# Kernel tuning notes

Hardware: AMD Instinct MI355X
Metric: run time of the kernel (lower is better)

The kernel has to match this reference:

```python
import jax, jax.numpy as jnp
import numpy as np

N_HEAD = 8
DQK = 64
DV = 64
D_IN = 512
D_OUT = 512
D_MID = 2048
B = 4
L = 2048
EPS = 1e-5


def layernorm(x):
    mu = jnp.mean(x, axis=-1, keepdims=True)
    var = jnp.mean(jnp.square(x - mu), axis=-1, keepdims=True)
    return (x - mu) / jnp.sqrt(var + EPS)


def setup_inputs() -> dict:
    key = jax.random.key(0)
    ks = jax.random.split(key, 10)
    s = 0.02
    return {
        "query": jax.random.normal(ks[0], (B, L, D_IN), jnp.float32),
        "key": jax.random.normal(ks[1], (B, L, D_IN), jnp.float32),
        "value": jax.random.normal(ks[2], (B, L, D_IN), jnp.float32),
        "mask": jnp.zeros((B, L, L), jnp.float32),
        "WQ": jax.random.normal(ks[3], (D_IN, N_HEAD * DQK), jnp.float32) * s,
        "WK": jax.random.normal(ks[4], (D_IN, N_HEAD * DQK), jnp.float32) * s,
        "WV": jax.random.normal(ks[5], (D_IN, N_HEAD * DV), jnp.float32) * s,
        "WO": jax.random.normal(ks[6], (N_HEAD * DV, D_OUT), jnp.float32) * s,
        "W1": jax.random.normal(ks[7], (D_OUT, D_MID), jnp.float32) * s,
        "W2": jax.random.normal(ks[8], (D_MID, D_OUT), jnp.float32) * s,
    }


def reference(query, key, value, mask, WQ, WK, WV, WO, W1, W2):
    bsz = query.shape[0]
    # projections -> [b, h, l, d]
    Q = (query @ WQ).reshape(bsz, -1, N_HEAD, DQK).transpose(0, 2, 1, 3)
    K = (key @ WK).reshape(bsz, -1, N_HEAD, DQK).transpose(0, 2, 1, 3)
    V = (value @ WV).reshape(bsz, -1, N_HEAD, DV).transpose(0, 2, 1, 3)
    # scaled dot-product attention with additive mask [b, 1, lq, lk]
    scores = jnp.einsum("bhqd,bhkd->bhqk", Q, K) / jnp.sqrt(jnp.float32(DQK))
    w = jax.nn.softmax(scores + mask[:, None, :, :], axis=-1)
    out = jnp.einsum("bhqk,bhkd->bhqd", w, V)
    out = out.transpose(0, 2, 1, 3).reshape(bsz, -1, N_HEAD * DV)
    out = out @ WO
    out = layernorm(query + out)
    ff = jax.nn.relu(out @ W1) @ W2
    return layernorm(out + ff)
```

## Files before the change

kernel.cpp:

```cpp
#include <hip/hip_runtime.h>
#include <hip/hip_bf16.h>

using bf16 = __bf16;
typedef __bf16 bf16x4 __attribute__((ext_vector_type(4)));
typedef __bf16 bf16x8 __attribute__((ext_vector_type(8)));
typedef float f32x4 __attribute__((ext_vector_type(4)));

static constexpr int BATCH = 4;
static constexpr int SEQ   = 2048;
static constexpr int DIN   = 512;
static constexpr int NHEAD = 8;
static constexpr int DMID  = 2048;
static constexpr int MROWS = BATCH * SEQ;

__device__ __forceinline__ void gload16(const void* g, void* l)
{
    __builtin_amdgcn_global_load_lds(
        (const __attribute__((address_space(1))) unsigned int*)g,
        (__attribute__((address_space(3))) unsigned int*)l, 16, 0, 0);
}

__global__ __launch_bounds__(256) void mask_check(const uint4* __restrict__ m,
                                                  int* __restrict__ flag)
{
    const int base = (blockIdx.x * 256 + threadIdx.x) * 4;
    unsigned nz = 0;
    for (int i = 0; i < 4; ++i) {
        const uint4 v = m[base + i];
        nz |= v.x | v.y | v.z | v.w;
    }
    if (nz) atomicOr(flag, 1);
}

__global__ __launch_bounds__(256) void transpose_weights(
    const float* __restrict__ WQ, const float* __restrict__ WK,
    const float* __restrict__ WV, const float* __restrict__ WO,
    const float* __restrict__ W1, const float* __restrict__ W2,
    bf16* __restrict__ WQt, bf16* __restrict__ WKt, bf16* __restrict__ WVt,
    bf16* __restrict__ WOt, bf16* __restrict__ W1t, bf16* __restrict__ W2t)
{
    __shared__ float tile[32][33];
    const int bid = blockIdx.x;
    const float* in; bf16* out; int ip, op, cx, ry;
    if (bid < 1024) {
        const int w = bid >> 8, idx = bid & 255;
        in  = w == 0 ? WQ  : w == 1 ? WK  : w == 2 ? WV  : WO;
        out = w == 0 ? WQt : w == 1 ? WKt : w == 2 ? WVt : WOt;
        ip = 512; op = 512; cx = idx & 15; ry = idx >> 4;
    } else if (bid < 2048) {
        const int idx = bid - 1024;
        in = W1; out = W1t; ip = 2048; op = 512; cx = idx & 63; ry = idx >> 6;
    } else {
        const int idx = bid - 2048;
        in = W2; out = W2t; ip = 512; op = 2048; cx = idx & 15; ry = idx >> 4;
    }
    const int c0 = cx * 32, r0 = ry * 32;
    const int tx = threadIdx.x & 31, ty = threadIdx.x >> 5;
    for (int i = 0; i < 32; i += 8)
        tile[ty + i][tx] = in[(size_t)(r0 + ty + i) * ip + c0 + tx];
    __syncthreads();
    for (int i = 0; i < 32; i += 8)
        out[(size_t)(c0 + ty + i) * op + r0 + tx] = (bf16)tile[tx][ty + i];
}

__global__ __launch_bounds__(256) void transpose_b2b(const bf16* __restrict__ in,
                                                     bf16* __restrict__ out,
                                                     int ip, int op)
{
    __shared__ bf16 tile[32][33];
    const int c0 = blockIdx.x * 32;
    const int r0 = blockIdx.y * 32;
    const int tx = threadIdx.x & 31;
    const int ty = threadIdx.x >> 5;
    for (int i = 0; i < 32; i += 8)
        tile[ty + i][tx] = in[(size_t)(r0 + ty + i) * ip + c0 + tx];
    __syncthreads();
    for (int i = 0; i < 32; i += 8)
        out[(size_t)(c0 + ty + i) * op + r0 + tx] = tile[tx][ty + i];
}

template <int ACT, bool AF32>
__device__ __forceinline__ void gemm128_body(const void* __restrict__ Ain,
                                             const bf16* __restrict__ Bt,
                                             bf16* __restrict__ C,
                                             int N, int K,
                                             bf16* sA, bf16* sB)
{
    const int t    = threadIdx.x;
    const int lane = t & 63;
    const int wave = t >> 6;
    const int wm   = wave >> 1;
    const int wn   = wave & 1;
    const int lr   = lane & 15;
    const int lq   = lane >> 4;

    const int m0 = blockIdx.y * 128;
    const int n0 = blockIdx.x * 128;

    const int srow = lane >> 3;
    const int scol = (lane & 7) * 8;

    f32x4 acc[4][4] = {};

    for (int k0 = 0; k0 < K; k0 += 64) {
        if constexpr (AF32) {
            const float* Af = (const float*)Ain;
            float4 fa[8];
#pragma unroll
            for (int i = 0; i < 4; ++i) {
                const float* p = Af + (size_t)(m0 + (wave * 4 + i) * 8 + srow) * K + k0 + scol;
                fa[2 * i]     = *reinterpret_cast<const float4*>(p);
                fa[2 * i + 1] = *reinterpret_cast<const float4*>(p + 4);
            }
            if (k0) __syncthreads();
#pragma unroll
            for (int i = 0; i < 4; ++i) {
                const int ch = wave * 4 + i;
                gload16(Bt + (size_t)(n0 + ch * 8 + srow) * K + k0 + scol, sB + ch * 512);
            }
#pragma unroll
            for (int i = 0; i < 4; ++i) {
                const int r = (wave * 4 + i) * 8 + srow;
                const float4 a = fa[2 * i], b = fa[2 * i + 1];
                bf16x8 h;
                h[0] = (bf16)a.x; h[1] = (bf16)a.y; h[2] = (bf16)a.z; h[3] = (bf16)a.w;
                h[4] = (bf16)b.x; h[5] = (bf16)b.y; h[6] = (bf16)b.z; h[7] = (bf16)b.w;
                *reinterpret_cast<bf16x8*>(&sA[r * 64 + scol]) = h;
            }
        } else {
            const bf16* Ab = (const bf16*)Ain;
            if (k0) __syncthreads();
#pragma unroll
            for (int i = 0; i < 4; ++i) {
                const int ch = wave * 4 + i;
                const int r  = ch * 8 + srow;
                gload16(Ab + (size_t)(m0 + r) * K + k0 + scol, sA + ch * 512);
                gload16(Bt + (size_t)(n0 + r) * K + k0 + scol, sB + ch * 512);
            }
        }
        __syncthreads();

#pragma unroll
        for (int kk = 0; kk < 2; ++kk) {
            bf16x8 af[4], bfr[4];
#pragma unroll
            for (int x = 0; x < 4; ++x) {
                af[x]  = *reinterpret_cast<const bf16x8*>(&sA[(wm * 64 + x * 16 + lr) * 64 + kk * 32 + lq * 8]);
                bfr[x] = *reinterpret_cast<const bf16x8*>(&sB[(wn * 64 + x * 16 + lr) * 64 + kk * 32 + lq * 8]);
            }
#pragma unroll
            for (int m = 0; m < 4; ++m)
#pragma unroll
                for (int n = 0; n < 4; ++n)
                    acc[m][n] = __builtin_amdgcn_mfma_f32_16x16x32_bf16(af[m], bfr[n], acc[m][n], 0, 0, 0);
        }
    }

#pragma unroll
    for (int n = 0; n < 4; ++n) {
        const int col = n0 + wn * 64 + n * 16 + lr;
#pragma unroll
        for (int m = 0; m < 4; ++m) {
            const int rowb = m0 + wm * 64 + m * 16 + lq * 4;
#pragma unroll
            for (int j = 0; j < 4; ++j) {
                float v = acc[m][n][j];
                if (ACT == 1) v = v > 0.f ? v : 0.f;
                C[(size_t)(rowb + j) * N + col] = (bf16)v;
            }
        }
    }
}

template <int ACT>
__global__ __launch_bounds__(256) void gemm128(const bf16* __restrict__ A,
                                               const bf16* __restrict__ Bt,
                                               bf16* __restrict__ C,
                                               int N, int K)
{
    __shared__ bf16 sA[128 * 64];
    __shared__ bf16 sB[128 * 64];
    gemm128_body<ACT, false>(A, Bt, C, N, K, sA, sB);
}

__global__ __launch_bounds__(256) void gemm128_qkv(const float* __restrict__ q,
                                                   const float* __restrict__ k,
                                                   const float* __restrict__ v,
                                                   const bf16* __restrict__ WQt,
                                                   const bf16* __restrict__ WKt,
                                                   const bf16* __restrict__ WVt,
                                                   bf16* __restrict__ Qb,
                                                   bf16* __restrict__ Kb,
                                                   bf16* __restrict__ Vb)
{
    __shared__ bf16 sA[128 * 64];
    __shared__ bf16 sB[128 * 64];
    const void* A  = blockIdx.z == 0 ? (const void*)q : blockIdx.z == 1 ? (const void*)k : (const void*)v;
    const bf16* Bt = blockIdx.z == 0 ? WQt : blockIdx.z == 1 ? WKt : WVt;
    bf16*       C  = blockIdx.z == 0 ? Qb  : blockIdx.z == 1 ? Kb  : Vb;
    gemm128_body<0, true>(A, Bt, C, DIN, DIN, sA, sB);
}

__global__ __launch_bounds__(256) void attn_kernel(const bf16* __restrict__ Qb,
                                                   const bf16* __restrict__ Kb,
                                                   const bf16* __restrict__ Vt,
                                                   const float* __restrict__ mask,
                                                   bf16* __restrict__ O,
                                                   const int* __restrict__ mzf)
{
    const int bi   = blockIdx.x;
    const int xcd  = bi & 7;
    const int slot = bi >> 3;
    const int pair = xcd * 4 + (slot >> 5);
    const int qt   = slot & 31;
    const int h    = pair >> 2;
    const int b    = pair & 3;

    const int t    = threadIdx.x;
    const int lane = t & 63;
    const int wave = t >> 6;
    const int lr   = lane & 15;
    const int lq   = lane >> 4;
    const int q0   = qt * 64;
    const bool useM = (*mzf != 0);

    __shared__ bf16 sK[64 * 72];
    __shared__ bf16 sV[64 * 72];
    __shared__ bf16 sP[4][16 * 72];
    __shared__ bf16 sM[64 * 68];

    const int  qrow = q0 + wave * 16 + lr;
    const bf16* qp  = Qb + (size_t)(b * SEQ + qrow) * DIN + h * 64 + lq * 8;
    const bf16x8 qf0 = *reinterpret_cast<const bf16x8*>(qp);
    const bf16x8 qf1 = *reinterpret_cast<const bf16x8*>(qp + 32);

    f32x4 o[4] = {};
    f32x4 lrow = {};

    const int sr = t >> 2;
    const int sc = (t & 3) << 3;

    const bf16*  kbase = Kb + (size_t)(b * SEQ) * DIN + h * 64;
    const bf16*  vbase = Vt + (size_t)(h * 64 + sr) * MROWS + b * SEQ;
    const float* mbase = mask + ((size_t)b * SEQ + q0) * SEQ;

    constexpr float L2E = 1.4426950408889634f;
    constexpr float SCL = 0.125f * L2E;
    const bf16x8 ones = {(bf16)1.f, (bf16)1.f, (bf16)1.f, (bf16)1.f,
                         (bf16)1.f, (bf16)1.f, (bf16)1.f, (bf16)1.f};

    int4 kr0 = *reinterpret_cast<const int4*>(kbase + (size_t)sr * DIN + sc);
    int4 kr1 = *reinterpret_cast<const int4*>(kbase + (size_t)sr * DIN + sc + 32);
    int4 vr0 = *reinterpret_cast<const int4*>(vbase + sc);
    int4 vr1 = *reinterpret_cast<const int4*>(vbase + sc + 32);

    for (int tile = 0; tile < SEQ / 64; ++tile) {
        if (tile) __syncthreads();

        *reinterpret_cast<int4*>(&sK[sr * 72 + sc])      = kr0;
        *reinterpret_cast<int4*>(&sK[sr * 72 + sc + 32]) = kr1;
        *reinterpret_cast<int4*>(&sV[sr * 72 + sc])      = vr0;
        *reinterpret_cast<int4*>(&sV[sr * 72 + sc + 32]) = vr1;
        if (useM) {
            const int k0 = tile * 64;
            for (int i = 0; i < 4; ++i) {
                const int idx = t + 256 * i;
                const float4 mr = *reinterpret_cast<const float4*>(
                    mbase + (size_t)(idx >> 4) * SEQ + k0 + (idx & 15) * 4);
                bf16x4 mv;
                mv[0] = (bf16)(mr.x * L2E); mv[1] = (bf16)(mr.y * L2E);
                mv[2] = (bf16)(mr.z * L2E); mv[3] = (bf16)(mr.w * L2E);
                *reinterpret_cast<bf16x4*>(&sM[(idx >> 4) * 68 + (idx & 15) * 4]) = mv;
            }
        }

        if (tile + 1 < SEQ / 64) {
            const int k0 = (tile + 1) * 64;
            kr0 = *reinterpret_cast<const int4*>(kbase + (size_t)(k0 + sr) * DIN + sc);
            kr1 = *reinterpret_cast<const int4*>(kbase + (size_t)(k0 + sr) * DIN + sc + 32);
            vr0 = *reinterpret_cast<const int4*>(vbase + k0 + sc);
            vr1 = *reinterpret_cast<const int4*>(vbase + k0 + sc + 32);
        }
        __syncthreads();

        f32x4 sf[4] = {};
        for (int s = 0; s < 2; ++s) {
            const bf16x8 qf = s ? qf1 : qf0;
            for (int ni = 0; ni < 4; ++ni) {
                bf16x8 kf = *reinterpret_cast<const bf16x8*>(&sK[(ni * 16 + lr) * 72 + s * 32 + lq * 8]);
                sf[ni] = __builtin_amdgcn_mfma_f32_16x16x32_bf16(qf, kf, sf[ni], 0, 0, 0);
            }
        }

        if (useM) {
            for (int j = 0; j < 4; ++j) {
                const int mr2 = (wave * 16 + lq * 4 + j) * 68;
                for (int ni = 0; ni < 4; ++ni) {
                    const float mval = (float)sM[mr2 + ni * 16 + lr];
                    sP[wave][(lq * 4 + j) * 72 + ni * 16 + lr] = (bf16)exp2f(sf[ni][j] * SCL + mval);
                }
            }
        } else {
            for (int j = 0; j < 4; ++j)
                for (int ni = 0; ni < 4; ++ni)
                    sP[wave][(lq * 4 + j) * 72 + ni * 16 + lr] = (bf16)exp2f(sf[ni][j] * SCL);
        }

        f32x4 rs = {};
        for (int s = 0; s < 2; ++s) {
            bf16x8 pf = *reinterpret_cast<const bf16x8*>(&sP[wave][lr * 72 + s * 32 + lq * 8]);
            rs = __builtin_amdgcn_mfma_f32_16x16x32_bf16(pf, ones, rs, 0, 0, 0);
            for (int ni = 0; ni < 4; ++ni) {
                bf16x8 vf = *reinterpret_cast<const bf16x8*>(&sV[(ni * 16 + lr) * 72 + s * 32 + lq * 8]);
                o[ni] = __builtin_amdgcn_mfma_f32_16x16x32_bf16(pf, vf, o[ni], 0, 0, 0);
            }
        }
        for (int j = 0; j < 4; ++j)
            lrow[j] += rs[j];
    }

    for (int ni = 0; ni < 4; ++ni)
        for (int j = 0; j < 4; ++j) {
            const int row = q0 + wave * 16 + lq * 4 + j;
            const int col = h * 64 + ni * 16 + lr;
            O[(size_t)(b * SEQ + row) * DIN + col] = (bf16)(o[ni][j] / lrow[j]);
        }
}

__global__ __launch_bounds__(256) void add_ln(const float* __restrict__ X,
                                              const bf16* __restrict__ Y,
                                              bf16* __restrict__ Ob,
                                              float* __restrict__ Of)
{
    const int row  = blockIdx.x * 4 + (threadIdx.x >> 6);
    const int lane = threadIdx.x & 63;
    const size_t base = (size_t)row * DIN + lane * 8;
    const float4 x0 = *reinterpret_cast<const float4*>(X + base);
    const float4 x1 = *reinterpret_cast<const float4*>(X + base + 4);
    const bf16x8 yv = *reinterpret_cast<const bf16x8*>(Y + base);
    float v[8] = {x0.x, x0.y, x0.z, x0.w, x1.x, x1.y, x1.z, x1.w};
    float s = 0.f;
    for (int i = 0; i < 8; ++i) { v[i] += (float)yv[i]; s += v[i]; }
    for (int off = 1; off < 64; off <<= 1) s += __shfl_xor(s, off);
    const float mu = s * (1.f / DIN);
    float var = 0.f;
    for (int i = 0; i < 8; ++i) { const float d = v[i] - mu; var += d * d; }
    for (int off = 1; off < 64; off <<= 1) var += __shfl_xor(var, off);
    const float rstd = rsqrtf(var * (1.f / DIN) + 1e-5f);
    float r[8];
    for (int i = 0; i < 8; ++i) r[i] = (v[i] - mu) * rstd;
    if (Ob) {
        bf16x8 ov;
        for (int i = 0; i < 8; ++i) ov[i] = (bf16)r[i];
        *reinterpret_cast<bf16x8*>(Ob + base) = ov;
    }
    if (Of) {
        *reinterpret_cast<float4*>(Of + base)     = make_float4(r[0], r[1], r[2], r[3]);
        *reinterpret_cast<float4*>(Of + base + 4) = make_float4(r[4], r[5], r[6], r[7]);
    }
}

extern "C" void kernel_launch(void* const* d_in, const int* in_sizes, int n_in,
                              void* d_out, int out_size, void* d_ws, size_t ws_size,
                              hipStream_t stream)
{
    const float* query = (const float*)d_in[0];
    const float* key   = (const float*)d_in[1];
    const float* value = (const float*)d_in[2];
    const float* mask  = (const float*)d_in[3];
    const float* WQ    = (const float*)d_in[4];
    const float* WK    = (const float*)d_in[5];
    const float* WV    = (const float*)d_in[6];
    const float* WO    = (const float*)d_in[7];
    const float* W1    = (const float*)d_in[8];
    const float* W2    = (const float*)d_in[9];

    char* w = (char*)d_ws;
    size_t off = 0;
    auto carve2 = [&](size_t elems) { bf16* p = (bf16*)(w + off); off += elems * 2; return p; };
    auto carve4 = [&](size_t elems) { float* p = (float*)(w + off); off += elems * 4; return p; };

    bf16* Qb    = carve2((size_t)MROWS * DIN);
    bf16* Kb    = carve2((size_t)MROWS * DIN);
    bf16* Vb    = carve2((size_t)MROWS * DIN);
    bf16* Vt    = carve2((size_t)MROWS * DIN);
    bf16* Mid   = carve2((size_t)MROWS * DMID);
    float* Ln1f = carve4((size_t)MROWS * DIN);
    bf16* WQt   = carve2((size_t)DIN * DIN);
    bf16* WKt   = carve2((size_t)DIN * DIN);
    bf16* WVt   = carve2((size_t)DIN * DIN);
    bf16* WOt   = carve2((size_t)DIN * DIN);
    bf16* W1t   = carve2((size_t)DIN * DMID);
    bf16* W2t   = carve2((size_t)DMID * DIN);
    int*  mzf   = (int*)(w + off); off += 16;
    if (off > ws_size) return;

    bf16* Ob   = Vb;
    bf16* Two  = Qb;
    bf16* Ln1b = Kb;
    bf16* F2   = Vt;

    const dim3 blk(256);

    hipMemsetAsync(mzf, 0, 4, stream);
    mask_check<<<dim3(4096), blk, 0, stream>>>((const uint4*)mask, mzf);

    transpose_weights<<<dim3(3072), blk, 0, stream>>>(WQ, WK, WV, WO, W1, W2,
                                                      WQt, WKt, WVt, WOt, W1t, W2t);

    gemm128_qkv<<<dim3(DIN / 128, MROWS / 128, 3), blk, 0, stream>>>(query, key, value,
                                                                     WQt, WKt, WVt, Qb, Kb, Vb);

    transpose_b2b<<<dim3(DIN / 32, MROWS / 32), blk, 0, stream>>>(Vb, Vt, DIN, MROWS);

    attn_kernel<<<dim3(1024), blk, 0, stream>>>(Qb, Kb, Vt, mask, Ob, mzf);

    gemm128<0><<<dim3(DIN / 128, MROWS / 128), blk, 0, stream>>>(Ob, WOt, Two, DIN, DIN);
    add_ln<<<dim3(MROWS / 4), blk, 0, stream>>>(query, Two, Ln1b, Ln1f);

    gemm128<1><<<dim3(DMID / 128, MROWS / 128), blk, 0, stream>>>(Ln1b, W1t, Mid, DMID, DIN);
    gemm128<0><<<dim3(DIN / 128, MROWS / 128), blk, 0, stream>>>(Mid, W2t, F2, DIN, DMID);

    add_ln<<<dim3(MROWS / 4), blk, 0, stream>>>(Ln1f, F2, (bf16*)nullptr, (float*)d_out);
}
```

Before: 372.7 us.

## Use 64-row GEMM tiles for narrow GEMMs and 128-query attention tiles

Adds a 64x128 GEMM variant used for the QKV projection, the output projection and the W2 GEMM. For N=512 outputs this doubles the block count, which improves occupancy across the many CUs. The attention kernel now gives each wave 32 query rows instead of 16. Each loaded K/V tile and its register fragments are then reused twice, and the grid is halved to 512 blocks. The trade-offs are higher register and LDS pressure in attention, and fewer attention blocks than the CU count may leave some CUs idle.

After: 367.6 us. No clear change (-1.4%).

```diff
diff --git a/kernel.cpp b/kernel.cpp
--- a/kernel.cpp
+++ b/kernel.cpp
@@ -79,13 +79,15 @@
         out[(size_t)(c0 + ty + i) * op + r0 + tx] = tile[tx][ty + i];
 }
 
-template <int ACT, bool AF32>
-__device__ __forceinline__ void gemm128_body(const void* __restrict__ Ain,
-                                             const bf16* __restrict__ Bt,
-                                             bf16* __restrict__ C,
-                                             int N, int K,
-                                             bf16* sA, bf16* sB)
-{
+template <int ACT>
+__global__ __launch_bounds__(256) void gemm128(const bf16* __restrict__ A,
+                                               const bf16* __restrict__ Bt,
+                                               bf16* __restrict__ C,
+                                               int N, int K)
+{
+    __shared__ bf16 sA[128 * 64];
+    __shared__ bf16 sB[128 * 64];
+
     const int t    = threadIdx.x;
     const int lane = t & 63;
     const int wave = t >> 6;
@@ -103,40 +105,13 @@
     f32x4 acc[4][4] = {};
 
     for (int k0 = 0; k0 < K; k0 += 64) {
-        if constexpr (AF32) {
-            const float* Af = (const float*)Ain;
-            float4 fa[8];
-#pragma unroll
-            for (int i = 0; i < 4; ++i) {
-                const float* p = Af + (size_t)(m0 + (wave * 4 + i) * 8 + srow) * K + k0 + scol;
-                fa[2 * i]     = *reinterpret_cast<const float4*>(p);
-                fa[2 * i + 1] = *reinterpret_cast<const float4*>(p + 4);
-            }
-            if (k0) __syncthreads();
-#pragma unroll
-            for (int i = 0; i < 4; ++i) {
-                const int ch = wave * 4 + i;
-                gload16(Bt + (size_t)(n0 + ch * 8 + srow) * K + k0 + scol, sB + ch * 512);
-            }
-#pragma unroll
-            for (int i = 0; i < 4; ++i) {
-                const int r = (wave * 4 + i) * 8 + srow;
-                const float4 a = fa[2 * i], b = fa[2 * i + 1];
-                bf16x8 h;
-                h[0] = (bf16)a.x; h[1] = (bf16)a.y; h[2] = (bf16)a.z; h[3] = (bf16)a.w;
-                h[4] = (bf16)b.x; h[5] = (bf16)b.y; h[6] = (bf16)b.z; h[7] = (bf16)b.w;
-                *reinterpret_cast<bf16x8*>(&sA[r * 64 + scol]) = h;
-            }
-        } else {
-            const bf16* Ab = (const bf16*)Ain;
-            if (k0) __syncthreads();
-#pragma unroll
-            for (int i = 0; i < 4; ++i) {
-                const int ch = wave * 4 + i;
-                const int r  = ch * 8 + srow;
-                gload16(Ab + (size_t)(m0 + r) * K + k0 + scol, sA + ch * 512);
-                gload16(Bt + (size_t)(n0 + r) * K + k0 + scol, sB + ch * 512);
-            }
+        if (k0) __syncthreads();
+#pragma unroll
+        for (int i = 0; i < 4; ++i) {
+            const int ch = wave * 4 + i;
+            const int r  = ch * 8 + srow;
+            gload16(A  + (size_t)(m0 + r) * K + k0 + scol, sA + ch * 512);
+            gload16(Bt + (size_t)(n0 + r) * K + k0 + scol, sB + ch * 512);
         }
         __syncthreads();
 
@@ -172,33 +147,128 @@
     }
 }
 
+template <int ACT, bool AF32>
+__device__ __forceinline__ void gemm64_body(const void* __restrict__ Ain,
+                                            const bf16* __restrict__ Bt,
+                                            bf16* __restrict__ C,
+                                            int N, int K,
+                                            bf16* sA, bf16* sB)
+{
+    const int t    = threadIdx.x;
+    const int lane = t & 63;
+    const int wave = t >> 6;
+    const int lr   = lane & 15;
+    const int lq   = lane >> 4;
+
+    const int m0 = blockIdx.y * 64;
+    const int n0 = blockIdx.x * 128;
+
+    const int srow = lane >> 3;
+    const int scol = (lane & 7) * 8;
+
+    f32x4 acc[4][2] = {};
+
+    for (int k0 = 0; k0 < K; k0 += 64) {
+        if constexpr (AF32) {
+            const float* Af = (const float*)Ain;
+            float4 fa[4];
+#pragma unroll
+            for (int i = 0; i < 2; ++i) {
+                const float* p = Af + (size_t)(m0 + (wave * 2 + i) * 8 + srow) * K + k0 + scol;
+                fa[2 * i]     = *reinterpret_cast<const float4*>(p);
+                fa[2 * i + 1] = *reinterpret_cast<const float4*>(p + 4);
+            }
+            if (k0) __syncthreads();
+#pragma unroll
+            for (int i = 0; i < 4; ++i) {
+                const int ch = wave * 4 + i;
+                gload16(Bt + (size_t)(n0 + ch * 8 + srow) * K + k0 + scol, sB + ch * 512);
+            }
+#pragma unroll
+            for (int i = 0; i < 2; ++i) {
+                const int r = (wave * 2 + i) * 8 + srow;
+                const float4 a = fa[2 * i], b = fa[2 * i + 1];
+                bf16x8 hh;
+                hh[0] = (bf16)a.x; hh[1] = (bf16)a.y; hh[2] = (bf16)a.z; hh[3] = (bf16)a.w;
+                hh[4] = (bf16)b.x; hh[5] = (bf16)b.y; hh[6] = (bf16)b.z; hh[7] = (bf16)b.w;
+                *reinterpret_cast<bf16x8*>(&sA[r * 64 + scol]) = hh;
+            }
+        } else {
+            const bf16* Ab = (const bf16*)Ain;
+            if (k0) __syncthreads();
+#pragma unroll
+            for (int i = 0; i < 2; ++i) {
+                const int ch = wave * 2 + i;
+                gload16(Ab + (size_t)(m0 + ch * 8 + srow) * K + k0 + scol, sA + ch * 512);
+            }
+#pragma unroll
+            for (int i = 0; i < 4; ++i) {
+                const int ch = wave * 4 + i;
+                gload16(Bt + (size_t)(n0 + ch * 8 + srow) * K + k0 + scol, sB + ch * 512);
+            }
+        }
+        __syncthreads();
+
+#pragma unroll
+        for (int kk = 0; kk < 2; ++kk) {
+            bf16x8 af[4], bfr[2];
+#pragma unroll
+            for (int x = 0; x < 4; ++x)
+                af[x] = *reinterpret_cast<const bf16x8*>(&sA[(x * 16 + lr) * 64 + kk * 32 + lq * 8]);
+#pragma unroll
+            for (int n = 0; n < 2; ++n)
+                bfr[n] = *reinterpret_cast<const bf16x8*>(&sB[(wave * 32 + n * 16 + lr) * 64 + kk * 32 + lq * 8]);
+#pragma unroll
+            for (int m = 0; m < 4; ++m)
+#pragma unroll
+                for (int n = 0; n < 2; ++n)
+                    acc[m][n] = __builtin_amdgcn_mfma_f32_16x16x32_bf16(af[m], bfr[n], acc[m][n], 0, 0, 0);
+        }
+    }
+
+#pragma unroll
+    for (int n = 0; n < 2; ++n) {
+        const int col = n0 + wave * 32 + n * 16 + lr;
+#pragma unroll
+        for (int m = 0; m < 4; ++m) {
+            const int rowb = m0 + m * 16 + lq * 4;
+#pragma unroll
+            for (int j = 0; j < 4; ++j) {
+                float v = acc[m][n][j];
+                if (ACT == 1) v = v > 0.f ? v : 0.f;
+                C[(size_t)(rowb + j) * N + col] = (bf16)v;
+            }
+        }
+    }
+}
+
 template <int ACT>
-__global__ __launch_bounds__(256) void gemm128(const bf16* __restrict__ A,
-                                               const bf16* __restrict__ Bt,
-                                               bf16* __restrict__ C,
-                                               int N, int K)
-{
-    __shared__ bf16 sA[128 * 64];
+__global__ __launch_bounds__(256) void gemm64(const bf16* __restrict__ A,
+                                              const bf16* __restrict__ Bt,
+                                              bf16* __restrict__ C,
+                                              int N, int K)
+{
+    __shared__ bf16 sA[64 * 64];
     __shared__ bf16 sB[128 * 64];
-    gemm128_body<ACT, false>(A, Bt, C, N, K, sA, sB);
-}
-
-__global__ __launch_bounds__(256) void gemm128_qkv(const float* __restrict__ q,
-                                                   const float* __restrict__ k,
-                                                   const float* __restrict__ v,
-                                                   const bf16* __restrict__ WQt,
-                                                   const bf16* __restrict__ WKt,
-                                                   const bf16* __restrict__ WVt,
-                                                   bf16* __restrict__ Qb,
-                                                   bf16* __restrict__ Kb,
-                                                   bf16* __restrict__ Vb)
-{
-    __shared__ bf16 sA[128 * 64];
+    gemm64_body<ACT, false>(A, Bt, C, N, K, sA, sB);
+}
+
+__global__ __launch_bounds__(256) void gemm64_qkv(const float* __restrict__ q,
+                                                  const float* __restrict__ k,
+                                                  const float* __restrict__ v,
+                                                  const bf16* __restrict__ WQt,
+                                                  const bf16* __restrict__ WKt,
+                                                  const bf16* __restrict__ WVt,
+                                                  bf16* __restrict__ Qb,
+                                                  bf16* __restrict__ Kb,
+                                                  bf16* __restrict__ Vb)
+{
+    __shared__ bf16 sA[64 * 64];
     __shared__ bf16 sB[128 * 64];
     const void* A  = blockIdx.z == 0 ? (const void*)q : blockIdx.z == 1 ? (const void*)k : (const void*)v;
     const bf16* Bt = blockIdx.z == 0 ? WQt : blockIdx.z == 1 ? WKt : WVt;
     bf16*       C  = blockIdx.z == 0 ? Qb  : blockIdx.z == 1 ? Kb  : Vb;
-    gemm128_body<0, true>(A, Bt, C, DIN, DIN, sA, sB);
+    gemm64_body<0, true>(A, Bt, C, DIN, DIN, sA, sB);
 }
 
 __global__ __launch_bounds__(256) void attn_kernel(const bf16* __restrict__ Qb,
@@ -211,8 +281,8 @@
     const int bi   = blockIdx.x;
     const int xcd  = bi & 7;
     const int slot = bi >> 3;
-    const int pair = xcd * 4 + (slot >> 5);
-    const int qt   = slot & 31;
+    const int pair = xcd * 4 + (slot >> 4);
+    const int qt   = slot & 15;
     const int h    = pair >> 2;
     const int b    = pair & 3;
 
@@ -221,21 +291,25 @@
     const int wave = t >> 6;
     const int lr   = lane & 15;
     const int lq   = lane >> 4;
-    const int q0   = qt * 64;
+    const int q0   = qt * 128;
     const bool useM = (*mzf != 0);
 
     __shared__ bf16 sK[64 * 72];
     __shared__ bf16 sV[64 * 72];
-    __shared__ bf16 sP[4][16 * 72];
-    __shared__ bf16 sM[64 * 68];
-
-    const int  qrow = q0 + wave * 16 + lr;
-    const bf16* qp  = Qb + (size_t)(b * SEQ + qrow) * DIN + h * 64 + lq * 8;
-    const bf16x8 qf0 = *reinterpret_cast<const bf16x8*>(qp);
-    const bf16x8 qf1 = *reinterpret_cast<const bf16x8*>(qp + 32);
-
-    f32x4 o[4] = {};
-    f32x4 lrow = {};
+    __shared__ bf16 sP[4][32 * 72];
+    __shared__ bf16 sM[128 * 68];
+
+    bf16x8 qf[2][2];
+#pragma unroll
+    for (int g = 0; g < 2; ++g) {
+        const int qrow = q0 + wave * 32 + g * 16 + lr;
+        const bf16* qp = Qb + (size_t)(b * SEQ + qrow) * DIN + h * 64 + lq * 8;
+        qf[g][0] = *reinterpret_cast<const bf16x8*>(qp);
+        qf[g][1] = *reinterpret_cast<const bf16x8*>(qp + 32);
+    }
+
+    f32x4 o[2][4] = {};
+    f32x4 lrow[2] = {};
 
     const int sr = t >> 2;
     const int sc = (t & 3) << 3;
@@ -263,7 +337,8 @@
         *reinterpret_cast<int4*>(&sV[sr * 72 + sc + 32]) = vr1;
         if (useM) {
             const int k0 = tile * 64;
-            for (int i = 0; i < 4; ++i) {
+#pragma unroll
+            for (int i = 0; i < 8; ++i) {
                 const int idx = t + 256 * i;
                 const float4 mr = *reinterpret_cast<const float4*>(
                     mbase + (size_t)(idx >> 4) * SEQ + k0 + (idx & 15) * 4);
@@ -283,48 +358,75 @@
         }
         __syncthreads();
 
-        f32x4 sf[4] = {};
-        for (int s = 0; s < 2; ++s) {
-            const bf16x8 qf = s ? qf1 : qf0;
-            for (int ni = 0; ni < 4; ++ni) {
-                bf16x8 kf = *reinterpret_cast<const bf16x8*>(&sK[(ni * 16 + lr) * 72 + s * 32 + lq * 8]);
-                sf[ni] = __builtin_amdgcn_mfma_f32_16x16x32_bf16(qf, kf, sf[ni], 0, 0, 0);
-            }
-        }
-
-        if (useM) {
+        bf16x8 kf[2][4];
+#pragma unroll
+        for (int s = 0; s < 2; ++s)
+#pragma unroll
+            for (int ni = 0; ni < 4; ++ni)
+                kf[s][ni] = *reinterpret_cast<const bf16x8*>(&sK[(ni * 16 + lr) * 72 + s * 32 + lq * 8]);
+
+#pragma unroll
+        for (int g = 0; g < 2; ++g) {
+            f32x4 sf[4] = {};
+#pragma unroll
+            for (int s = 0; s < 2; ++s)
+#pragma unroll
+                for (int ni = 0; ni < 4; ++ni)
+                    sf[ni] = __builtin_amdgcn_mfma_f32_16x16x32_bf16(qf[g][s], kf[s][ni], sf[ni], 0, 0, 0);
+
+            if (useM) {
+#pragma unroll
+                for (int j = 0; j < 4; ++j) {
+                    const int mr2 = (wave * 32 + g * 16 + lq * 4 + j) * 68;
+#pragma unroll
+                    for (int ni = 0; ni < 4; ++ni) {
+                        const float mval = (float)sM[mr2 + ni * 16 + lr];
+                        sP[wave][(g * 16 + lq * 4 + j) * 72 + ni * 16 + lr] = (bf16)exp2f(sf[ni][j] * SCL + mval);
+                    }
+                }
+            } else {
+#pragma unroll
+                for (int j = 0; j < 4; ++j)
+#pragma unroll
+                    for (int ni = 0; ni < 4; ++ni)
+                        sP[wave][(g * 16 + lq * 4 + j) * 72 + ni * 16 + lr] = (bf16)exp2f(sf[ni][j] * SCL);
+            }
+        }
+
+        bf16x8 vf[2][4];
+#pragma unroll
+        for (int s = 0; s < 2; ++s)
+#pragma unroll
+            for (int ni = 0; ni < 4; ++ni)
+                vf[s][ni] = *reinterpret_cast<const bf16x8*>(&sV[(ni * 16 + lr) * 72 + s * 32 + lq * 8]);
+
+#pragma unroll
+        for (int g = 0; g < 2; ++g) {
+            f32x4 rs = {};
+#pragma unroll
+            for (int s = 0; s < 2; ++s) {
+                bf16x8 pf = *reinterpret_cast<const bf16x8*>(&sP[wave][(g * 16 + lr) * 72 + s * 32 + lq * 8]);
+                rs = __builtin_amdgcn_mfma_f32_16x16x32_bf16(pf, ones, rs, 0, 0, 0);
+#pragma unroll
+                for (int ni = 0; ni < 4; ++ni)
+                    o[g][ni] = __builtin_amdgcn_mfma_f32_16x16x32_bf16(pf, vf[s][ni], o[g][ni], 0, 0, 0);
+            }
+#pragma unroll
+            for (int j = 0; j < 4; ++j)
+                lrow[g][j] += rs[j];
+        }
+    }
+
+#pragma unroll
+    for (int g = 0; g < 2; ++g)
+#pragma unroll
+        for (int ni = 0; ni < 4; ++ni)
+#pragma unroll
             for (int j = 0; j < 4; ++j) {
-                const int mr2 = (wave * 16 + lq * 4 + j) * 68;
-                for (int ni = 0; ni < 4; ++ni) {
-                    const float mval = (float)sM[mr2 + ni * 16 + lr];
-                    sP[wave][(lq * 4 + j) * 72 + ni * 16 + lr] = (bf16)exp2f(sf[ni][j] * SCL + mval);
-                }
-            }
-        } else {
-            for (int j = 0; j < 4; ++j)
-                for (int ni = 0; ni < 4; ++ni)
-                    sP[wave][(lq * 4 + j) * 72 + ni * 16 + lr] = (bf16)exp2f(sf[ni][j] * SCL);
-        }
-
-        f32x4 rs = {};
-        for (int s = 0; s < 2; ++s) {
-            bf16x8 pf = *reinterpret_cast<const bf16x8*>(&sP[wave][lr * 72 + s * 32 + lq * 8]);
-            rs = __builtin_amdgcn_mfma_f32_16x16x32_bf16(pf, ones, rs, 0, 0, 0);
-            for (int ni = 0; ni < 4; ++ni) {
-                bf16x8 vf = *reinterpret_cast<const bf16x8*>(&sV[(ni * 16 + lr) * 72 + s * 32 + lq * 8]);
-                o[ni] = __builtin_amdgcn_mfma_f32_16x16x32_bf16(pf, vf, o[ni], 0, 0, 0);
-            }
-        }
-        for (int j = 0; j < 4; ++j)
-            lrow[j] += rs[j];
-    }
-
-    for (int ni = 0; ni < 4; ++ni)
-        for (int j = 0; j < 4; ++j) {
-            const int row = q0 + wave * 16 + lq * 4 + j;
-            const int col = h * 64 + ni * 16 + lr;
-            O[(size_t)(b * SEQ + row) * DIN + col] = (bf16)(o[ni][j] / lrow[j]);
-        }
+                const int row = q0 + wave * 32 + g * 16 + lq * 4 + j;
+                const int col = h * 64 + ni * 16 + lr;
+                O[(size_t)(b * SEQ + row) * DIN + col] = (bf16)(o[g][ni][j] / lrow[g][j]);
+            }
 }
 
 __global__ __launch_bounds__(256) void add_ln(const float* __restrict__ X,
@@ -408,18 +510,18 @@
     transpose_weights<<<dim3(3072), blk, 0, stream>>>(WQ, WK, WV, WO, W1, W2,
                                                       WQt, WKt, WVt, WOt, W1t, W2t);
 
-    gemm128_qkv<<<dim3(DIN / 128, MROWS / 128, 3), blk, 0, stream>>>(query, key, value,
-                                                                     WQt, WKt, WVt, Qb, Kb, Vb);
+    gemm64_qkv<<<dim3(DIN / 128, MROWS / 64, 3), blk, 0, stream>>>(query, key, value,
+                                                                   WQt, WKt, WVt, Qb, Kb, Vb);
 
     transpose_b2b<<<dim3(DIN / 32, MROWS / 32), blk, 0, stream>>>(Vb, Vt, DIN, MROWS);
 
-    attn_kernel<<<dim3(1024), blk, 0, stream>>>(Qb, Kb, Vt, mask, Ob, mzf);
-
-    gemm128<0><<<dim3(DIN / 128, MROWS / 128), blk, 0, stream>>>(Ob, WOt, Two, DIN, DIN);
+    attn_kernel<<<dim3(512), blk, 0, stream>>>(Qb, Kb, Vt, mask, Ob, mzf);
+
+    gemm64<0><<<dim3(DIN / 128, MROWS / 64), blk, 0, stream>>>(Ob, WOt, Two, DIN, DIN);
     add_ln<<<dim3(MROWS / 4), blk, 0, stream>>>(query, Two, Ln1b, Ln1f);
 
     gemm128<1><<<dim3(DMID / 128, MROWS / 128), blk, 0, stream>>>(Ln1b, W1t, Mid, DMID, DIN);
-    gemm128<0><<<dim3(DIN / 128, MROWS / 128), blk, 0, stream>>>(Mid, W2t, F2, DIN, DMID);
+    gemm64<0><<<dim3(DIN / 128, MROWS / 64), blk, 0, stream>>>(Mid, W2t, F2, DIN, DMID);
 
     add_ln<<<dim3(MROWS / 4), blk, 0, stream>>>(Ln1f, F2, (bf16*)nullptr, (float*)d_out);
 }
```
